# Kernel optimization log

Measured on AMD Instinct MI355X. Metric: run time of the kernel, lower is better.

Reference implementation:

```python
import jax, jax.numpy as jnp
import numpy as np

B, S, D = 2, 4096, 1024
H = 16
HD = D // H  # 64


def setup_inputs() -> dict:
    key = jax.random.key(0)
    ks = jax.random.split(key, 5)
    scale = 1.0 / np.sqrt(D)
    return {
        "x": jax.random.normal(ks[0], (B, S, D), dtype=jnp.float32),
        "Wq": jax.random.normal(ks[1], (D, D), dtype=jnp.float32) * scale,
        "Wk": jax.random.normal(ks[2], (D, D), dtype=jnp.float32) * scale,
        "Wv": jax.random.normal(ks[3], (D, D), dtype=jnp.float32) * scale,
        "Wo": jax.random.normal(ks[4], (D, D), dtype=jnp.float32) * scale,
        "bo": jnp.zeros((D,), dtype=jnp.float32),
    }


def reference(x, Wq, Wk, Wv, Wo, bo):
    b, s, d = x.shape
    # Linear layers (torch layout: weight [out, in], y = x @ W.T)
    q = (x @ Wq.T).reshape(b, s, H, HD)
    k = (x @ Wk.T).reshape(b, s, H, HD)
    v = (x @ Wv.T).reshape(b, s, H, HD)
    # scores: [b, h, q, k]
    scores = jnp.einsum("bqhd,bkhd->bhqk", q, k)
    # causal mask (upper triangle above diagonal -> -inf)
    causal = jnp.triu(jnp.ones((s, s), dtype=bool), k=1)
    scores = jnp.where(causal[None, None], -jnp.inf, scores)
    weights = jax.nn.softmax(scores / np.sqrt(HD), axis=-1)  # dropout p=0.0 -> identity
    ctx = jnp.einsum("bhqk,bkhd->bqhd", weights, v).reshape(b, s, d)
    return ctx @ Wo.T + bo
```

## Files before the change

### kernel.cpp

```cpp
#include <hip/hip_runtime.h>
#include <stdint.h>
#include <stddef.h>

#define S_LEN 4096
#define NHEAD 16
#define HDIM 64
#define DMODEL 1024
#define NBATCH 2
#define LOG2E 1.4426950408889634f

typedef __attribute__((ext_vector_type(8))) short bf16x8;
typedef __attribute__((ext_vector_type(4))) float f32x4;
typedef __attribute__((ext_vector_type(16))) float f32x16;
typedef __attribute__((ext_vector_type(2))) unsigned int uint2v;
typedef __attribute__((ext_vector_type(4))) unsigned int uint4v;

__device__ inline unsigned short f2b(float f) {
    union { float f; unsigned int u; } x; x.f = f;
    unsigned int r = (x.u + 0x7fffu + ((x.u >> 16) & 1u)) >> 16;
    return (unsigned short)r;
}

__device__ inline unsigned cvt_pk_bf16(float lo, float hi) {
    unsigned r;
    asm("v_cvt_pk_bf16_f32 %0, %1, %2" : "=v"(r) : "v"(lo), "v"(hi));
    return r;
}

__device__ inline float exp_fast(float x) {
    float r;
    asm("v_exp_f32 %0, %1" : "=v"(r) : "v"(x));
    return r;
}

__device__ inline void gload_lds16(const void* g, void* l) {
    __builtin_amdgcn_global_load_lds((const __attribute__((address_space(1))) void*)g,
                                     (__attribute__((address_space(3))) void*)l,
                                     16, 0, 0);
}

__global__ void cvt_x(const float* __restrict__ in, unsigned short* __restrict__ out, int n4) {
    int i = blockIdx.x * 256 + threadIdx.x;
    if (i >= n4) return;
    float4 v = ((const float4*)in)[i];
    ushort4 o;
    o.x = f2b(v.x); o.y = f2b(v.y); o.z = f2b(v.z); o.w = f2b(v.w);
    ((ushort4*)out)[i] = o;
}

__global__ void cvt_w(const float* __restrict__ w0, const float* __restrict__ w1,
                      const float* __restrict__ w2, const float* __restrict__ w3,
                      unsigned short* __restrict__ dst) {
    int z = blockIdx.y;
    const float* src = (z == 0) ? w0 : (z == 1) ? w1 : (z == 2) ? w2 : w3;
    int i = blockIdx.x * 256 + threadIdx.x;
    float4 v = ((const float4*)src)[i];
    ushort4 o;
    o.x = f2b(v.x); o.y = f2b(v.y); o.z = f2b(v.z); o.w = f2b(v.w);
    ((ushort4*)(dst + (size_t)z * DMODEL * DMODEL))[i] = o;
}

__global__ __launch_bounds__(256, 2)
void gemm_qkv(const unsigned short* __restrict__ xb,
              const unsigned short* __restrict__ wqb,
              const unsigned short* __restrict__ wkb,
              const unsigned short* __restrict__ wvb,
              unsigned short* __restrict__ Qb,
              unsigned short* __restrict__ Kb,
              unsigned short* __restrict__ Vt,
              float qscale) {
    __shared__ unsigned short Asl[128 * 64];
    __shared__ unsigned short Bsl[128 * 64];
    const int tid  = threadIdx.x;
    const int lane = tid & 63;
    const int wid  = tid >> 6;
    const int wm   = (wid >> 1) * 64, wn = (wid & 1) * 64;
    const int lr   = lane & 15, lk = lane >> 4;
    const int z    = blockIdx.z;

    const unsigned short* A;
    const unsigned short* Bw;
    int m0, n0;
    if (z < 2) { A = xb; Bw = z ? wkb : wqb; m0 = blockIdx.x * 128; n0 = blockIdx.y * 128; }
    else       { A = wvb; Bw = xb;           m0 = blockIdx.y * 128; n0 = blockIdx.x * 128; }

    f32x4 acc[4][4];
#pragma unroll
    for (int i = 0; i < 4; ++i)
#pragma unroll
        for (int j = 0; j < 4; ++j) acc[i][j] = (f32x4){0.f, 0.f, 0.f, 0.f};

    for (int kt = 0; kt < DMODEL; kt += 64) {
#pragma unroll
        for (int i = 0; i < 4; ++i) {
            int c = i * 256 + tid;
            int r = c >> 3, gc = (c & 7) ^ (r & 7);
            gload_lds16(A + (size_t)(m0 + r) * DMODEL + kt + gc * 8, Asl + c * 8);
        }
#pragma unroll
        for (int i = 0; i < 4; ++i) {
            int c = i * 256 + tid;
            int r = c >> 3, gc = (c & 7) ^ (r & 7);
            gload_lds16(Bw + (size_t)(n0 + r) * DMODEL + kt + gc * 8, Bsl + c * 8);
        }
        __syncthreads();
#pragma unroll
        for (int kh = 0; kh < 2; ++kh) {
            int cl = kh * 4 + lk;
            bf16x8 af[4], bfr[4];
#pragma unroll
            for (int m = 0; m < 4; ++m) {
                int r = wm + m * 16 + lr;
                af[m] = *(const bf16x8*)(Asl + r * 64 + ((cl ^ (r & 7)) * 8));
            }
#pragma unroll
            for (int n = 0; n < 4; ++n) {
                int r = wn + n * 16 + lr;
                bfr[n] = *(const bf16x8*)(Bsl + r * 64 + ((cl ^ (r & 7)) * 8));
            }
#pragma unroll
            for (int m = 0; m < 4; ++m)
#pragma unroll
                for (int n = 0; n < 4; ++n)
                    acc[m][n] = __builtin_amdgcn_mfma_f32_16x16x32_bf16(af[m], bfr[n], acc[m][n], 0, 0, 0);
        }
        __syncthreads();
    }

#pragma unroll
    for (int m = 0; m < 4; ++m) {
#pragma unroll
        for (int n = 0; n < 4; ++n) {
            int gn = n0 + wn + n * 16 + lr;
#pragma unroll
            for (int r = 0; r < 4; ++r) {
                int gm = m0 + wm + m * 16 + lk * 4 + r;
                float v = acc[m][n][r];
                if (z == 0) {
                    int b = gm >> 12, s = gm & 4095, h = gn >> 6, hd = gn & 63;
                    Qb[((size_t)((b * NHEAD + h) * S_LEN + s)) * HDIM + hd] = f2b(v * qscale);
                } else if (z == 1) {
                    int b = gm >> 12, s = gm & 4095, h = gn >> 6, hd = gn & 63;
                    Kb[((size_t)((b * NHEAD + h) * S_LEN + s)) * HDIM + hd] = f2b(v);
                } else {
                    int h = gm >> 6, hd = gm & 63, b = gn >> 12, s = gn & 4095;
                    Vt[((size_t)((b * NHEAD + h) * HDIM + hd)) * S_LEN + s] = f2b(v);
                }
            }
        }
    }
}

__global__ __launch_bounds__(256, 2)
void gemm_out(const unsigned short* __restrict__ A,
              const unsigned short* __restrict__ Bw,
              float* __restrict__ out, const float* __restrict__ bias) {
    __shared__ unsigned short Asl[128 * 64];
    __shared__ unsigned short Bsl[128 * 64];
    const int tid  = threadIdx.x;
    const int lane = tid & 63;
    const int wid  = tid >> 6;
    const int wm   = (wid >> 1) * 64, wn = (wid & 1) * 64;
    const int lr   = lane & 15, lk = lane >> 4;
    const int m0   = blockIdx.x * 128, n0 = blockIdx.y * 128;

    f32x4 acc[4][4];
#pragma unroll
    for (int i = 0; i < 4; ++i)
#pragma unroll
        for (int j = 0; j < 4; ++j) acc[i][j] = (f32x4){0.f, 0.f, 0.f, 0.f};

    for (int kt = 0; kt < DMODEL; kt += 64) {
#pragma unroll
        for (int i = 0; i < 4; ++i) {
            int c = i * 256 + tid;
            int r = c >> 3, gc = (c & 7) ^ (r & 7);
            gload_lds16(A + (size_t)(m0 + r) * DMODEL + kt + gc * 8, Asl + c * 8);
        }
#pragma unroll
        for (int i = 0; i < 4; ++i) {
            int c = i * 256 + tid;
            int r = c >> 3, gc = (c & 7) ^ (r & 7);
            gload_lds16(Bw + (size_t)(n0 + r) * DMODEL + kt + gc * 8, Bsl + c * 8);
        }
        __syncthreads();
#pragma unroll
        for (int kh = 0; kh < 2; ++kh) {
            int cl = kh * 4 + lk;
            bf16x8 af[4], bfr[4];
#pragma unroll
            for (int m = 0; m < 4; ++m) {
                int r = wm + m * 16 + lr;
                af[m] = *(const bf16x8*)(Asl + r * 64 + ((cl ^ (r & 7)) * 8));
            }
#pragma unroll
            for (int n = 0; n < 4; ++n) {
                int r = wn + n * 16 + lr;
                bfr[n] = *(const bf16x8*)(Bsl + r * 64 + ((cl ^ (r & 7)) * 8));
            }
#pragma unroll
            for (int m = 0; m < 4; ++m)
#pragma unroll
                for (int n = 0; n < 4; ++n)
                    acc[m][n] = __builtin_amdgcn_mfma_f32_16x16x32_bf16(af[m], bfr[n], acc[m][n], 0, 0, 0);
        }
        __syncthreads();
    }
#pragma unroll
    for (int m = 0; m < 4; ++m)
#pragma unroll
        for (int n = 0; n < 4; ++n) {
            int gn = n0 + wn + n * 16 + lr;
#pragma unroll
            for (int r = 0; r < 4; ++r) {
                int gm = m0 + wm + m * 16 + lk * 4 + r;
                out[(size_t)gm * DMODEL + gn] = acc[m][n][r] + bias[gn];
            }
        }
}

__global__ __launch_bounds__(256)
void attn_fwd(const unsigned short* __restrict__ Q,
              const unsigned short* __restrict__ K,
              const unsigned short* __restrict__ Vt,
              unsigned short* __restrict__ ctx) {
    __shared__ unsigned short Kl[2][4096];
    __shared__ unsigned short Vl[2][4096];

    const int tid  = threadIdx.x;
    const int lane = tid & 63;
    const int w    = tid >> 6;
    const int l31  = lane & 31;
    const int hi   = lane >> 5;

    const int bid  = blockIdx.x;
    const int xcd  = bid & 7;
    const int cu   = (bid >> 3) & 31;
    const int slot = bid >> 8;
    const int u    = cu >> 2;
    int qt;
    if      (slot == 0) qt = 31 - u;
    else if (slot == 1) qt = 16 + u;
    else if (slot == 2) qt = 15 - u;
    else                qt = u;
    const int bh   = (xcd << 2) | (cu & 3);
    const int b    = bh >> 4, h = bh & 15;
    const int q0   = qt * 128;
    const int qw0  = q0 + w * 32;

    const unsigned short* Qh = Q  + (size_t)bh * S_LEN * HDIM;
    const unsigned short* Kh = K  + (size_t)bh * S_LEN * HDIM;
    const unsigned short* Vh = Vt + (size_t)bh * HDIM * S_LEN;

    const int skA  = tid >> 6;
    const int lS   = tid & 63;
    const int lS31 = lS & 31, hiS = lS >> 5;
    const unsigned short* kb0 = Kh + (size_t)lS31 * HDIM + skA * 16 + hiS * 8;
    const unsigned short* kb1 = Kh + (size_t)(32 + lS31) * HDIM + skA * 16 + hiS * 8;
    const unsigned short* vb0 = Vh + (size_t)lS31 * S_LEN + skA * 16 + hiS * 8;
    const unsigned short* vb1 = Vh + (size_t)(32 + lS31) * S_LEN + skA * 16 + hiS * 8;

    bf16x8 qf[4];
    {
        const unsigned short* qrow = Qh + (size_t)(qw0 + l31) * HDIM + hi * 8;
#pragma unroll
        for (int s = 0; s < 4; ++s) qf[s] = *(const bf16x8*)(qrow + s * 16);
    }

    bf16x8 ones;
#pragma unroll
    for (int j = 0; j < 8; ++j) ones[j] = (short)0x3F80;

    f32x16 z16;
#pragma unroll
    for (int j = 0; j < 16; ++j) z16[j] = 0.f;

    const unsigned short* KL = &Kl[0][0] + lane * 8;
    const unsigned short* VL = &Vl[0][0] + lane * 8;

    f32x16 o0, o1, ls;
#pragma unroll
    for (int j = 0; j < 16; ++j) { o0[j] = 0.f; o1[j] = 0.f; ls[j] = 0.f; }

    const int nt = 2 * qt + 2;

    auto stage = [&](int buf, int kv0) {
        gload_lds16(kb0 + (size_t)kv0 * HDIM, &Kl[buf][(size_t)tid * 8]);
        gload_lds16(kb1 + (size_t)kv0 * HDIM, &Kl[buf][2048 + (size_t)tid * 8]);
        gload_lds16(vb0 + kv0, &Vl[buf][(size_t)tid * 8]);
        gload_lds16(vb1 + kv0, &Vl[buf][2048 + (size_t)tid * 8]);
    };

    auto packfrag = [&](const f32x16& v, int base) -> bf16x8 {
        unsigned a0 = cvt_pk_bf16(v[base + 0], v[base + 1]), a1 = cvt_pk_bf16(v[base + 2], v[base + 3]);
        unsigned b0 = cvt_pk_bf16(v[base + 4], v[base + 5]), b1 = cvt_pk_bf16(v[base + 6], v[base + 7]);
        uint2v r0 = __builtin_amdgcn_permlane32_swap(a0, b0, false, false);
        uint2v r1 = __builtin_amdgcn_permlane32_swap(a1, b1, false, false);
        uint4v f; f.x = r0.x; f.y = r1.x; f.z = r0.y; f.w = r1.y;
        return __builtin_bit_cast(bf16x8, f);
    };

    auto compute = [&](int buf, int kv0) {
        const unsigned short* KB = KL + buf * 4096;
        const unsigned short* VB = VL + buf * 4096;
        const int q = qw0 + l31;

        if (kv0 < qw0 + 32) {
            __builtin_amdgcn_s_setprio(1);
            f32x16 st = __builtin_amdgcn_mfma_f32_32x32x16_bf16(
                            *(const bf16x8*)(KB + 0 * 512), qf[0], z16, 0, 0, 0);
#pragma unroll
            for (int s = 1; s < 4; ++s)
                st = __builtin_amdgcn_mfma_f32_32x32x16_bf16(
                        *(const bf16x8*)(KB + s * 512), qf[s], st, 0, 0, 0);
            __builtin_amdgcn_s_setprio(0);
            if (kv0 + 31 > qw0) {
#pragma unroll
                for (int j = 0; j < 16; ++j) {
                    int roff = (j & 3) + 8 * (j >> 2) + 4 * hi;
                    if (kv0 + roff > q) st[j] = -3e38f;
                }
            }
#pragma unroll
            for (int j = 0; j < 16; ++j) st[j] = exp_fast(st[j]);
            bf16x8 pa = packfrag(st, 0);
            bf16x8 pb = packfrag(st, 8);
            __builtin_amdgcn_s_setprio(1);
            ls = __builtin_amdgcn_mfma_f32_32x32x16_bf16(ones, pa, ls, 0, 0, 0);
            ls = __builtin_amdgcn_mfma_f32_32x32x16_bf16(ones, pb, ls, 0, 0, 0);
            o0 = __builtin_amdgcn_mfma_f32_32x32x16_bf16(*(const bf16x8*)(VB + 0 * 512), pa, o0, 0, 0, 0);
            o1 = __builtin_amdgcn_mfma_f32_32x32x16_bf16(*(const bf16x8*)(VB + 4 * 512), pa, o1, 0, 0, 0);
            o0 = __builtin_amdgcn_mfma_f32_32x32x16_bf16(*(const bf16x8*)(VB + 1 * 512), pb, o0, 0, 0, 0);
            o1 = __builtin_amdgcn_mfma_f32_32x32x16_bf16(*(const bf16x8*)(VB + 5 * 512), pb, o1, 0, 0, 0);
            __builtin_amdgcn_s_setprio(0);
        }

        if (kv0 < qw0) {
            __builtin_amdgcn_s_setprio(1);
            f32x16 st = __builtin_amdgcn_mfma_f32_32x32x16_bf16(
                            *(const bf16x8*)(KB + 4 * 512), qf[0], z16, 0, 0, 0);
#pragma unroll
            for (int s = 1; s < 4; ++s)
                st = __builtin_amdgcn_mfma_f32_32x32x16_bf16(
                        *(const bf16x8*)(KB + (4 + s) * 512), qf[s], st, 0, 0, 0);
            __builtin_amdgcn_s_setprio(0);
            if (kv0 + 63 > qw0) {
#pragma unroll
                for (int j = 0; j < 16; ++j) {
                    int roff = (j & 3) + 8 * (j >> 2) + 4 * hi;
                    if (kv0 + 32 + roff > q) st[j] = -3e38f;
                }
            }
#pragma unroll
            for (int j = 0; j < 16; ++j) st[j] = exp_fast(st[j]);
            bf16x8 pa = packfrag(st, 0);
            bf16x8 pb = packfrag(st, 8);
            __builtin_amdgcn_s_setprio(1);
            ls = __builtin_amdgcn_mfma_f32_32x32x16_bf16(ones, pa, ls, 0, 0, 0);
            ls = __builtin_amdgcn_mfma_f32_32x32x16_bf16(ones, pb, ls, 0, 0, 0);
            o0 = __builtin_amdgcn_mfma_f32_32x32x16_bf16(*(const bf16x8*)(VB + 2 * 512), pa, o0, 0, 0, 0);
            o1 = __builtin_amdgcn_mfma_f32_32x32x16_bf16(*(const bf16x8*)(VB + 6 * 512), pa, o1, 0, 0, 0);
            o0 = __builtin_amdgcn_mfma_f32_32x32x16_bf16(*(const bf16x8*)(VB + 3 * 512), pb, o0, 0, 0, 0);
            o1 = __builtin_amdgcn_mfma_f32_32x32x16_bf16(*(const bf16x8*)(VB + 7 * 512), pb, o1, 0, 0, 0);
            __builtin_amdgcn_s_setprio(0);
        }
    };

    stage(0, 0);
    __syncthreads();
    for (int t = 0; t < nt; t += 2) {
        const int kv0 = t * 64;
        stage(1, kv0 + 64);
        compute(0, kv0);
        __syncthreads();
        if (t + 2 < nt) stage(0, kv0 + 128);
        compute(1, kv0 + 64);
        __syncthreads();
    }

    float inv = 1.f / ls[0];
    size_t sq = (size_t)q0 + w * 32 + l31;
    unsigned short* crow = ctx + ((size_t)b * S_LEN + sq) * DMODEL + h * HDIM;
#pragma unroll
    for (int quad = 0; quad < 4; ++quad) {
        int hdbase = quad * 8 + hi * 4;
        unsigned w0 = cvt_pk_bf16(o0[4 * quad] * inv, o0[4 * quad + 1] * inv);
        unsigned w1 = cvt_pk_bf16(o0[4 * quad + 2] * inv, o0[4 * quad + 3] * inv);
        *(unsigned long long*)(crow + hdbase) = ((unsigned long long)w1 << 32) | w0;
        unsigned w2 = cvt_pk_bf16(o1[4 * quad] * inv, o1[4 * quad + 1] * inv);
        unsigned w3 = cvt_pk_bf16(o1[4 * quad + 2] * inv, o1[4 * quad + 3] * inv);
        *(unsigned long long*)(crow + 32 + hdbase) = ((unsigned long long)w3 << 32) | w2;
    }
}

extern "C" void kernel_launch(void* const* d_in, const int* in_sizes, int n_in,
                              void* d_out, int out_size, void* d_ws, size_t ws_size,
                              hipStream_t stream) {
    (void)in_sizes; (void)n_in; (void)out_size; (void)ws_size;
    const float* x  = (const float*)d_in[0];
    const float* Wq = (const float*)d_in[1];
    const float* Wk = (const float*)d_in[2];
    const float* Wv = (const float*)d_in[3];
    const float* Wo = (const float*)d_in[4];
    const float* bo = (const float*)d_in[5];

    unsigned short* ws  = (unsigned short*)d_ws;
    const size_t NTOK = (size_t)NBATCH * S_LEN;
    unsigned short* xb  = ws;
    unsigned short* wqb = xb  + NTOK * DMODEL;
    unsigned short* wkb = wqb + (size_t)DMODEL * DMODEL;
    unsigned short* wvb = wkb + (size_t)DMODEL * DMODEL;
    unsigned short* wob = wvb + (size_t)DMODEL * DMODEL;
    unsigned short* Qb  = wob + (size_t)DMODEL * DMODEL;
    unsigned short* Kb  = Qb  + NTOK * DMODEL;
    unsigned short* Vt  = Kb  + NTOK * DMODEL;
    unsigned short* ctx = xb;

    int n4x = (int)(NTOK * DMODEL / 4);
    cvt_x<<<(n4x + 255) / 256, 256, 0, stream>>>(x, xb, n4x);
    cvt_w<<<dim3(DMODEL * DMODEL / 4 / 256, 4), 256, 0, stream>>>(Wq, Wk, Wv, Wo, wqb);

    const float qscale = 0.125f * LOG2E;
    gemm_qkv<<<dim3(64, 8, 3), 256, 0, stream>>>(xb, wqb, wkb, wvb, Qb, Kb, Vt, qscale);

    attn_fwd<<<1024, 256, 0, stream>>>(Qb, Kb, Vt, ctx);

    gemm_out<<<dim3(64, 8), 256, 0, stream>>>(ctx, wob, (float*)d_out, bo);
}
```

Measured before the change: 193.8 us.

## Store K in MFMA fragment order and load it directly from global

The QKV GEMM now writes K in a pre-swizzled layout that matches the MFMA operand fragment order for each 64-key tile. The attention kernel then reads K fragments straight from global memory (through cache) instead of staging them into LDS, which halves the LDS staging traffic and shared-memory footprint. The cost is that K loads now sit on the compute critical path as global loads with latency that is not covered by the double-buffered prefetch, and the GEMM epilogue writes K with a scattered pattern.

```diff
diff --git a/kernel.cpp b/kernel.cpp
--- a/kernel.cpp
+++ b/kernel.cpp
@@ -66,7 +66,7 @@
               const unsigned short* __restrict__ wkb,
               const unsigned short* __restrict__ wvb,
               unsigned short* __restrict__ Qb,
-              unsigned short* __restrict__ Kb,
+              unsigned short* __restrict__ Kf,
               unsigned short* __restrict__ Vt,
               float qscale) {
     __shared__ unsigned short Asl[128 * 64];
@@ -140,8 +140,13 @@
                     int b = gm >> 12, s = gm & 4095, h = gn >> 6, hd = gn & 63;
                     Qb[((size_t)((b * NHEAD + h) * S_LEN + s)) * HDIM + hd] = f2b(v * qscale);
                 } else if (z == 1) {
-                    int b = gm >> 12, s = gm & 4095, h = gn >> 6, hd = gn & 63;
-                    Kb[((size_t)((b * NHEAD + h) * S_LEN + s)) * HDIM + hd] = f2b(v);
+                    int b = gm >> 12, kv = gm & 4095, h = gn >> 6, hd = gn & 63;
+                    int bh = b * NHEAD + h;
+                    int t64 = kv >> 6, half = (kv >> 5) & 1, l31k = kv & 31;
+                    int s = hd >> 4, hik = (hd >> 3) & 1, e = hd & 7;
+                    size_t idx = (((((size_t)bh * 64 + t64) * 2 + half) * 4 + s) * 64
+                                  + (hik * 32 + l31k)) * 8 + e;
+                    Kf[idx] = f2b(v);
                 } else {
                     int h = gm >> 6, hd = gm & 63, b = gn >> 12, s = gn & 4095;
                     Vt[((size_t)((b * NHEAD + h) * HDIM + hd)) * S_LEN + s] = f2b(v);
@@ -221,10 +226,9 @@
 
 __global__ __launch_bounds__(256)
 void attn_fwd(const unsigned short* __restrict__ Q,
-              const unsigned short* __restrict__ K,
+              const unsigned short* __restrict__ Kf,
               const unsigned short* __restrict__ Vt,
               unsigned short* __restrict__ ctx) {
-    __shared__ unsigned short Kl[2][4096];
     __shared__ unsigned short Vl[2][4096];
 
     const int tid  = threadIdx.x;
@@ -248,17 +252,14 @@
     const int q0   = qt * 128;
     const int qw0  = q0 + w * 32;
 
-    const unsigned short* Qh = Q  + (size_t)bh * S_LEN * HDIM;
-    const unsigned short* Kh = K  + (size_t)bh * S_LEN * HDIM;
-    const unsigned short* Vh = Vt + (size_t)bh * HDIM * S_LEN;
-
-    const int skA  = tid >> 6;
-    const int lS   = tid & 63;
-    const int lS31 = lS & 31, hiS = lS >> 5;
-    const unsigned short* kb0 = Kh + (size_t)lS31 * HDIM + skA * 16 + hiS * 8;
-    const unsigned short* kb1 = Kh + (size_t)(32 + lS31) * HDIM + skA * 16 + hiS * 8;
-    const unsigned short* vb0 = Vh + (size_t)lS31 * S_LEN + skA * 16 + hiS * 8;
-    const unsigned short* vb1 = Vh + (size_t)(32 + lS31) * S_LEN + skA * 16 + hiS * 8;
+    const unsigned short* Qh  = Q  + (size_t)bh * S_LEN * HDIM;
+    const unsigned short* Kfh = Kf + (size_t)bh * 64 * 2 * 2048;
+    const unsigned short* Vh  = Vt + (size_t)bh * HDIM * S_LEN;
+
+    const int sk   = tid >> 6;
+    const int lS31 = tid & 31, hiS = (tid >> 5) & 1;
+    const unsigned short* vb0 = Vh + (size_t)lS31 * S_LEN + sk * 16 + hiS * 8;
+    const unsigned short* vb1 = Vh + (size_t)(32 + lS31) * S_LEN + sk * 16 + hiS * 8;
 
     bf16x8 qf[4];
     {
@@ -275,8 +276,8 @@
 #pragma unroll
     for (int j = 0; j < 16; ++j) z16[j] = 0.f;
 
-    const unsigned short* KL = &Kl[0][0] + lane * 8;
     const unsigned short* VL = &Vl[0][0] + lane * 8;
+    const unsigned short* KFL = Kfh + lane * 8;
 
     f32x16 o0, o1, ls;
 #pragma unroll
@@ -285,8 +286,6 @@
     const int nt = 2 * qt + 2;
 
     auto stage = [&](int buf, int kv0) {
-        gload_lds16(kb0 + (size_t)kv0 * HDIM, &Kl[buf][(size_t)tid * 8]);
-        gload_lds16(kb1 + (size_t)kv0 * HDIM, &Kl[buf][2048 + (size_t)tid * 8]);
         gload_lds16(vb0 + kv0, &Vl[buf][(size_t)tid * 8]);
         gload_lds16(vb1 + kv0, &Vl[buf][2048 + (size_t)tid * 8]);
     };
@@ -301,18 +300,20 @@
     };
 
     auto compute = [&](int buf, int kv0) {
-        const unsigned short* KB = KL + buf * 4096;
         const unsigned short* VB = VL + buf * 4096;
         const int q = qw0 + l31;
 
         if (kv0 < qw0 + 32) {
+            const unsigned short* kb = KFL + ((size_t)(kv0 >> 6) * 2 + 0) * 2048;
+            bf16x8 k0 = *(const bf16x8*)(kb + 0 * 512);
+            bf16x8 k1 = *(const bf16x8*)(kb + 1 * 512);
+            bf16x8 k2 = *(const bf16x8*)(kb + 2 * 512);
+            bf16x8 k3 = *(const bf16x8*)(kb + 3 * 512);
             __builtin_amdgcn_s_setprio(1);
-            f32x16 st = __builtin_amdgcn_mfma_f32_32x32x16_bf16(
-                            *(const bf16x8*)(KB + 0 * 512), qf[0], z16, 0, 0, 0);
-#pragma unroll
-            for (int s = 1; s < 4; ++s)
-                st = __builtin_amdgcn_mfma_f32_32x32x16_bf16(
-                        *(const bf16x8*)(KB + s * 512), qf[s], st, 0, 0, 0);
+            f32x16 st = __builtin_amdgcn_mfma_f32_32x32x16_bf16(k0, qf[0], z16, 0, 0, 0);
+            st = __builtin_amdgcn_mfma_f32_32x32x16_bf16(k1, qf[1], st, 0, 0, 0);
+            st = __builtin_amdgcn_mfma_f32_32x32x16_bf16(k2, qf[2], st, 0, 0, 0);
+            st = __builtin_amdgcn_mfma_f32_32x32x16_bf16(k3, qf[3], st, 0, 0, 0);
             __builtin_amdgcn_s_setprio(0);
             if (kv0 + 31 > qw0) {
 #pragma unroll
@@ -336,13 +337,16 @@
         }
 
         if (kv0 < qw0) {
+            const unsigned short* kb = KFL + ((size_t)(kv0 >> 6) * 2 + 1) * 2048;
+            bf16x8 k0 = *(const bf16x8*)(kb + 0 * 512);
+            bf16x8 k1 = *(const bf16x8*)(kb + 1 * 512);
+            bf16x8 k2 = *(const bf16x8*)(kb + 2 * 512);
+            bf16x8 k3 = *(const bf16x8*)(kb + 3 * 512);
             __builtin_amdgcn_s_setprio(1);
-            f32x16 st = __builtin_amdgcn_mfma_f32_32x32x16_bf16(
-                            *(const bf16x8*)(KB + 4 * 512), qf[0], z16, 0, 0, 0);
-#pragma unroll
-            for (int s = 1; s < 4; ++s)
-                st = __builtin_amdgcn_mfma_f32_32x32x16_bf16(
-                        *(const bf16x8*)(KB + (4 + s) * 512), qf[s], st, 0, 0, 0);
+            f32x16 st = __builtin_amdgcn_mfma_f32_32x32x16_bf16(k0, qf[0], z16, 0, 0, 0);
+            st = __builtin_amdgcn_mfma_f32_32x32x16_bf16(k1, qf[1], st, 0, 0, 0);
+            st = __builtin_amdgcn_mfma_f32_32x32x16_bf16(k2, qf[2], st, 0, 0, 0);
+            st = __builtin_amdgcn_mfma_f32_32x32x16_bf16(k3, qf[3], st, 0, 0, 0);
             __builtin_amdgcn_s_setprio(0);
             if (kv0 + 63 > qw0) {
 #pragma unroll
@@ -412,8 +416,8 @@
     unsigned short* wvb = wkb + (size_t)DMODEL * DMODEL;
     unsigned short* wob = wvb + (size_t)DMODEL * DMODEL;
     unsigned short* Qb  = wob + (size_t)DMODEL * DMODEL;
-    unsigned short* Kb  = Qb  + NTOK * DMODEL;
-    unsigned short* Vt  = Kb  + NTOK * DMODEL;
+    unsigned short* Kfr = Qb  + NTOK * DMODEL;
+    unsigned short* Vt  = Kfr + NTOK * DMODEL;
     unsigned short* ctx = xb;
 
     int n4x = (int)(NTOK * DMODEL / 4);
@@ -421,9 +425,9 @@
     cvt_w<<<dim3(DMODEL * DMODEL / 4 / 256, 4), 256, 0, stream>>>(Wq, Wk, Wv, Wo, wqb);
 
     const float qscale = 0.125f * LOG2E;
-    gemm_qkv<<<dim3(64, 8, 3), 256, 0, stream>>>(xb, wqb, wkb, wvb, Qb, Kb, Vt, qscale);
-
-    attn_fwd<<<1024, 256, 0, stream>>>(Qb, Kb, Vt, ctx);
+    gemm_qkv<<<dim3(64, 8, 3), 256, 0, stream>>>(xb, wqb, wkb, wvb, Qb, Kfr, Vt, qscale);
+
+    attn_fwd<<<1024, 256, 0, stream>>>(Qb, Kfr, Vt, ctx);
 
     gemm_out<<<dim3(64, 8), 256, 0, stream>>>(ctx, wob, (float*)d_out, bo);
 }
```

Result: slower. 206.7 us (+6.7%).
